# Kernel tuning notes

Hardware: AMD Instinct MI355X
Metric: run time of the kernel (lower is better)

## Reference

```python
import jax, jax.numpy as jnp
import numpy as np

C = 512

def conv1x1(x, w, b):
    # x: [B,C,H,W], w: [O,C], b: [O]
    return jnp.einsum('bchw,oc->bohw', x, w) + b[None, :, None, None]

def setup_inputs() -> dict:
    key = jax.random.key(0)
    ks = jax.random.split(key, 7)
    s = 1.0 / np.sqrt(C)
    x = jax.random.normal(ks[0], (8, C, 64, 64), dtype=jnp.float32)
    wq = jax.random.uniform(ks[1], (C, C), jnp.float32, -s, s)
    bq = jax.random.uniform(ks[2], (C,), jnp.float32, -s, s)
    wk = jax.random.uniform(ks[3], (C, C), jnp.float32, -s, s)
    bk = jax.random.uniform(ks[4], (C,), jnp.float32, -s, s)
    wv = jax.random.uniform(ks[5], (C, C), jnp.float32, -s, s)
    bv = jax.random.uniform(ks[6], (C,), jnp.float32, -s, s)
    return {"x": x, "wq": wq, "bq": bq, "wk": wk, "bk": bk, "wv": wv, "bv": bv}

def reference(x, wq, bq, wk, bk, wv, bv):
    B, Cc, H, W = x.shape
    q = conv1x1(x, wq, bq).reshape(B, Cc, H * W)   # [B,C,N]
    k = conv1x1(x, wk, bk).reshape(B, Cc, H * W)   # [B,C,N]
    v = conv1x1(x, wv, bv).reshape(B, Cc, H * W)   # [B,C,N]
    attn = jnp.einsum('bcn,bdn->bcd', q, k)        # q @ k^T over spatial dim -> [B,C,C]
    attn = jax.nn.softmax(attn, axis=-1)
    out = jnp.einsum('bcd,bdn->bcn', attn, v).reshape(B, Cc, H, W)
    return out + x
```

## Files before the change

### kernel.cpp

```cpp
#include <hip/hip_runtime.h>
#include <cstdint>

typedef unsigned short u16;
typedef unsigned int   u32;
typedef _Float16 f16;

typedef __attribute__((ext_vector_type(8))) _Float16 f16x8;
typedef __attribute__((ext_vector_type(4))) float    f32x4;

__device__ __forceinline__ u16 f2h(float f) {
    union { f16 h; u16 u; } c; c.h = (f16)f; return c.u;
}
__device__ __forceinline__ float h2f(u16 u) {
    union { u16 u; f16 h; } c; c.u = u; return (float)c.h;
}

__device__ __forceinline__ void async_copy16(const u16* g, u16* lds) {
    __builtin_amdgcn_global_load_lds(
        (const __attribute__((address_space(1))) void*)g,
        (__attribute__((address_space(3))) void*)lds,
        16, 0, 0);
}

__device__ __forceinline__ void gemm_nt_f16(
    u16* smem, const u16* __restrict__ A, int lda,
    const u16* __restrict__ B, int ldb, int K, f32x4 acc[4][4])
{
    const int t = threadIdx.x, w = t >> 6, lane = t & 63;
    const int srow = lane >> 2;
    const int skc  = (((lane & 3) ^ ((lane >> 3) & 3)) * 8);
    const int ra0 = (w*2+0)*16 + srow, ra1 = (w*2+1)*16 + srow;
    const u16* gA0 = A + (size_t)ra0 * lda + skc;
    const u16* gA1 = A + (size_t)ra1 * lda + skc;
    const u16* gB0 = B + (size_t)ra0 * ldb + skc;
    const u16* gB1 = B + (size_t)ra1 * ldb + skc;
    u16* lA0 = smem + (w*2+0)*512;
    u16* lA1 = smem + (w*2+1)*512;
    const int fr = lane & 15, fq = lane >> 4;
    const int fc = (fq ^ ((fr >> 1) & 3)) * 8;
    const int wm = (w >> 1) * 64, wn = (w & 1) * 64;
    const int fAo = (wm + fr) * 32 + fc;
    const int fBo = (wn + fr) * 32 + fc;

    for (int k0 = 0; k0 < K; k0 += 64) {
        async_copy16(gA0 + k0,      lA0);
        async_copy16(gA1 + k0,      lA1);
        async_copy16(gA0 + k0 + 32, lA0 + 4096);
        async_copy16(gA1 + k0 + 32, lA1 + 4096);
        async_copy16(gB0 + k0,      lA0 + 8192);
        async_copy16(gB1 + k0,      lA1 + 8192);
        async_copy16(gB0 + k0 + 32, lA0 + 12288);
        async_copy16(gB1 + k0 + 32, lA1 + 12288);
        __syncthreads();
        {
            f16x8 af[4], bf[4];
#pragma unroll
            for (int i = 0; i < 4; i++) af[i] = *(const f16x8*)(smem + fAo + i * 512);
#pragma unroll
            for (int i = 0; i < 4; i++) bf[i] = *(const f16x8*)(smem + 8192 + fBo + i * 512);
#pragma unroll
            for (int mi = 0; mi < 4; mi++)
#pragma unroll
                for (int ni = 0; ni < 4; ni++)
                    acc[mi][ni] = __builtin_amdgcn_mfma_f32_16x16x32_f16(
                        af[mi], bf[ni], acc[mi][ni], 0, 0, 0);
        }
        {
            f16x8 af[4], bf[4];
#pragma unroll
            for (int i = 0; i < 4; i++) af[i] = *(const f16x8*)(smem + 4096 + fAo + i * 512);
#pragma unroll
            for (int i = 0; i < 4; i++) bf[i] = *(const f16x8*)(smem + 12288 + fBo + i * 512);
#pragma unroll
            for (int mi = 0; mi < 4; mi++)
#pragma unroll
                for (int ni = 0; ni < 4; ni++)
                    acc[mi][ni] = __builtin_amdgcn_mfma_f32_16x16x32_f16(
                        af[mi], bf[ni], acc[mi][ni], 0, 0, 0);
        }
        __syncthreads();
    }
}

__device__ __forceinline__ void zero_acc(f32x4 acc[4][4]) {
#pragma unroll
    for (int i = 0; i < 4; i++)
#pragma unroll
        for (int j = 0; j < 4; j++) {
            f32x4 z = {0.f, 0.f, 0.f, 0.f};
            acc[i][j] = z;
        }
}

__global__ __launch_bounds__(256) void k_prep(const float* __restrict__ wq,
                                              const float* __restrict__ wk,
                                              const float* __restrict__ wv,
                                              u16* __restrict__ Wq2,
                                              u16* __restrict__ Wkh,
                                              u16* __restrict__ WvT,
                                              float* __restrict__ s)
{
    if (blockIdx.x < 512) {
        const int t = blockIdx.x * 256 + threadIdx.x;
        if (t < 4096) s[t] = 0.f;
        const int e = t * 4;
        const int sel = e >> 18;
        const int off = e & 262143;
        const float* src = sel ? wk : wq;
        float4 v = *(const float4*)(src + off);
        ushort4 h;
        h.x = f2h(v.x); h.y = f2h(v.y); h.z = f2h(v.z); h.w = f2h(v.w);
        if (sel == 0) {
            int i = off >> 9, c = off & 511;
            *(ushort4*)(Wq2 + (size_t)i * 1024 + c) = h;
            *(ushort4*)(Wq2 + (size_t)i * 1024 + 512 + c) = h;
        } else {
            *(ushort4*)(Wkh + off) = h;
        }
    } else {
        __shared__ u16 tile[64][70];
        const int bx = blockIdx.x - 512;
        const int t = threadIdx.x;
        const int d0 = (bx >> 3) * 64;
        const int c0 = (bx & 7) * 64;
        const int rr = t >> 4, col4 = (t & 15) * 4;
#pragma unroll
        for (int i = 0; i < 4; i++) {
            int row = i * 16 + rr;
            float4 v = *(const float4*)(wv + (size_t)(d0 + row) * 512 + c0 + col4);
            ushort4 h;
            h.x = f2h(v.x); h.y = f2h(v.y); h.z = f2h(v.z); h.w = f2h(v.w);
            *(ushort4*)&tile[row][col4] = h;
        }
        __syncthreads();
#pragma unroll
        for (int i = 0; i < 4; i++) {
            int crow = i * 16 + rr;
            ushort4 o;
            o.x = tile[col4 + 0][crow];
            o.y = tile[col4 + 1][crow];
            o.z = tile[col4 + 2][crow];
            o.w = tile[col4 + 3][crow];
            *(ushort4*)(WvT + (size_t)(c0 + crow) * 512 + d0 + col4) = o;
        }
    }
}

__global__ __launch_bounds__(256) void k_convx(const float* __restrict__ x,
                                               u16* __restrict__ Xh,
                                               u16* __restrict__ XT,
                                               float* __restrict__ s)
{
    __shared__ u16 tile[64][70];
    const int t  = threadIdx.x;
    const int b  = blockIdx.z;
    const int c0 = blockIdx.y * 64;
    const int n0 = blockIdx.x * 64;
    const int rr   = t >> 4;
    const int col4 = (t & 15) * 4;

    const float* src = x + ((size_t)b * 512 + c0) * 4096 + n0;
    u16* xh = Xh + ((size_t)b * 512 + c0) * 4096 + n0;
#pragma unroll
    for (int i = 0; i < 4; i++) {
        int row = i * 16 + rr;
        float4 v = *(const float4*)(src + (size_t)row * 4096 + col4);
        ushort4 h;
        h.x = f2h(v.x); h.y = f2h(v.y); h.z = f2h(v.z); h.w = f2h(v.w);
        *(ushort4*)&tile[row][col4] = h;
        *(ushort4*)(xh + (size_t)row * 4096 + col4) = h;
        float p = v.x + v.y + v.z + v.w;
        p += __shfl_xor(p, 1); p += __shfl_xor(p, 2);
        p += __shfl_xor(p, 4); p += __shfl_xor(p, 8);
        if ((t & 15) == 0) atomicAdd(&s[b * 512 + c0 + row], p);
    }
    __syncthreads();
    u16* dst = XT + ((size_t)b * 4096 + n0) * 512 + c0;
#pragma unroll
    for (int i = 0; i < 4; i++) {
        int nrow = i * 16 + rr;
        ushort4 o;
        o.x = tile[col4 + 0][nrow];
        o.y = tile[col4 + 1][nrow];
        o.z = tile[col4 + 2][nrow];
        o.w = tile[col4 + 3][nrow];
        *(ushort4*)(dst + (size_t)nrow * 512 + col4) = o;
    }
}

__global__ __launch_bounds__(256, 4) void k_gram(const u16* __restrict__ Xh,
                                                 float* __restrict__ Gp)
{
    __shared__ u16 smem[16384];
    const int flat = blockIdx.x;
    const int swz  = (flat & 7) * 40 + (flat >> 3);
    const int tI = swz % 10;
    const int bz = swz / 10;
    const int tm = (tI >= 9) ? 3 : (tI >= 7) ? 2 : (tI >= 4) ? 1 : 0;
    const int rs = (tm == 0) ? 0 : (tm == 1) ? 4 : (tm == 2) ? 7 : 9;
    const int tn = tI - rs + tm;
    const int m0 = tm * 128, n0 = tn * 128;
    const int b  = bz >> 2, ks = bz & 3;

    const u16* Ap = Xh + (size_t)b * 512 * 4096 + (size_t)m0 * 4096 + ks * 1024;
    const u16* Bp = Xh + (size_t)b * 512 * 4096 + (size_t)n0 * 4096 + ks * 1024;

    f32x4 acc[4][4];
    zero_acc(acc);
    gemm_nt_f16(smem, Ap, 4096, Bp, 4096, 1024, acc);

    const int t = threadIdx.x, w = t >> 6, lane = t & 63;
    const int wm = (w >> 1) * 64, wn = (w & 1) * 64;
    const int cn = lane & 15, cq = lane >> 4;

    float* base = Gp + (size_t)(ks * 8 + b) * 512 * 512;
    float* outp = base + (size_t)m0 * 512 + n0;
#pragma unroll
    for (int mi = 0; mi < 4; mi++)
#pragma unroll
        for (int ni = 0; ni < 4; ni++)
#pragma unroll
            for (int r = 0; r < 4; r++) {
                int m = wm + mi * 16 + cq * 4 + r;
                int n = wn + ni * 16 + cn;
                outp[(size_t)m * 512 + n] = acc[mi][ni][r];
            }
    if (m0 != n0) {
        float* outT = base + (size_t)n0 * 512 + m0;
#pragma unroll
        for (int mi = 0; mi < 4; mi++)
#pragma unroll
            for (int ni = 0; ni < 4; ni++) {
                int mb = wm + mi * 16 + cq * 4;
                int n  = wn + ni * 16 + cn;
                float4 v4 = { acc[mi][ni][0], acc[mi][ni][1],
                              acc[mi][ni][2], acc[mi][ni][3] };
                *(float4*)(outT + (size_t)n * 512 + mb) = v4;
            }
    }
}

__global__ __launch_bounds__(256) void k_gred(const float* __restrict__ Gp,
                                              u16* __restrict__ Ghl,
                                              const float* __restrict__ wq,
                                              const float* __restrict__ bq,
                                              const float* __restrict__ wk,
                                              const float* __restrict__ s,
                                              float* __restrict__ ubar,
                                              float* __restrict__ vv)
{
    const size_t idx = ((size_t)blockIdx.x * 256 + threadIdx.x) * 4;
    const size_t st = (size_t)8 * 512 * 512;
    float4 g0 = *(const float4*)(Gp + idx);
    float4 g1 = *(const float4*)(Gp + idx + st);
    float4 g2 = *(const float4*)(Gp + idx + 2 * st);
    float4 g3 = *(const float4*)(Gp + idx + 3 * st);
    float gx = g0.x + g1.x + g2.x + g3.x;
    float gy = g0.y + g1.y + g2.y + g3.y;
    float gz = g0.z + g1.z + g2.z + g3.z;
    float gw = g0.w + g1.w + g2.w + g3.w;
    ushort4 hi, lo;
    hi.x = f2h(gx); lo.x = f2h(gx - h2f(hi.x));
    hi.y = f2h(gy); lo.y = f2h(gy - h2f(hi.y));
    hi.z = f2h(gz); lo.z = f2h(gz - h2f(hi.z));
    hi.w = f2h(gw); lo.w = f2h(gw - h2f(hi.w));
    const size_t row = idx >> 9;
    const int c = (int)(idx & 511);
    *(ushort4*)(Ghl + row * 1024 + c) = hi;
    *(ushort4*)(Ghl + row * 1024 + 512 + c) = lo;

    if (blockIdx.x < 128) {
        const int b = blockIdx.x >> 4;
        const int sub = blockIdx.x & 15;
        const int which = sub >> 3;
        const int r0 = (sub & 7) * 64;
        const int t = threadIdx.x;
        const int i = r0 + (t >> 2), l4 = t & 3;
        const float* W = which ? wk : wq;
        const float* sb = s + b * 512;
        float acc = 0.f;
#pragma unroll 4
        for (int k = 0; k < 32; k++) {
            int c2 = k * 16 + l4 * 4;
            float4 w4 = *(const float4*)(W + (size_t)i * 512 + c2);
            float4 s4 = *(const float4*)(sb + c2);
            acc += w4.x * s4.x + w4.y * s4.y + w4.z * s4.z + w4.w * s4.w;
        }
        acc += __shfl_xor(acc, 1);
        acc += __shfl_xor(acc, 2);
        if (l4 == 0) {
            if (which) vv[b * 512 + i] = acc;
            else       ubar[b * 512 + i] = acc + 4096.0f * bq[i];
        }
    }
}

__global__ __launch_bounds__(256, 4) void k_T(const u16* __restrict__ Wq2,
                                              const u16* __restrict__ Ghl,
                                              u16* __restrict__ Tb)
{
    __shared__ u16 smem[16384];
    const int n0 = blockIdx.x * 128;
    const int m0 = blockIdx.y * 128;
    const int b  = blockIdx.z;

    const u16* Ap = Wq2 + (size_t)m0 * 1024;
    const u16* Bp = Ghl + (size_t)b * 512 * 1024 + (size_t)n0 * 1024;

    f32x4 acc[4][4];
    zero_acc(acc);
    gemm_nt_f16(smem, Ap, 1024, Bp, 1024, 1024, acc);

    const int t = threadIdx.x, w = t >> 6, lane = t & 63;
    const int wm = (w >> 1) * 64, wn = (w & 1) * 64;
    const int cn = lane & 15, cq = lane >> 4;

    u16* outp = Tb + ((size_t)b * 512 + m0) * 512 + n0;
#pragma unroll
    for (int mi = 0; mi < 4; mi++)
#pragma unroll
        for (int ni = 0; ni < 4; ni++)
#pragma unroll
            for (int r = 0; r < 4; r++) {
                int m = wm + mi * 16 + cq * 4 + r;
                int n = wn + ni * 16 + cn;
                outp[(size_t)m * 512 + n] = f2h(acc[mi][ni][r]);
            }
}

__global__ __launch_bounds__(256) void k_S(
    const u16* __restrict__ Tb, const u16* __restrict__ Wkh,
    const float* __restrict__ ubar, const float* __restrict__ vv,
    const float* __restrict__ bq, const float* __restrict__ bk,
    const float* __restrict__ bv,
    u16* __restrict__ P, float* __restrict__ pbv)
{
    __shared__ u16 smem[16896];
    __shared__ float redm[16][4];
    __shared__ float reds[16][4][2];
    u16* As = smem; u16* Bs = smem + 512;

    const int m0 = blockIdx.x * 16;
    const int b  = blockIdx.y;
    const int t = threadIdx.x, w = t >> 6, lane = t & 63;
    const int srow = lane >> 2;
    const int schunk = ((lane & 3) ^ ((srow >> 1) & 3)) * 8;
    const u16* gA = Tb + ((size_t)b * 512 + m0 + srow) * 512 + schunk;
    const int fr = lane & 15, fq = lane >> 4;
    const int fc = (fq ^ ((fr >> 1) & 3)) * 8;

    f32x4 acc[8];
#pragma unroll
    for (int i = 0; i < 8; i++) { f32x4 z = {0.f,0.f,0.f,0.f}; acc[i] = z; }

    for (int k0 = 0; k0 < 512; k0 += 32) {
        if (w == 0) async_copy16(gA + k0, As);
#pragma unroll
        for (int ii = 0; ii < 8; ii++) {
            int rbase = w * 128 + ii * 16;
            async_copy16(Wkh + (size_t)(rbase + srow) * 512 + k0 + schunk,
                         Bs + rbase * 32);
        }
        __syncthreads();
        f16x8 af = *(const f16x8*)(As + fr * 32 + fc);
#pragma unroll
        for (int ni = 0; ni < 8; ni++) {
            f16x8 bf = *(const f16x8*)(Bs + (w * 128 + ni * 16 + fr) * 32 + fc);
            acc[ni] = __builtin_amdgcn_mfma_f32_16x16x32_f16(af, bf, acc[ni], 0, 0, 0);
        }
        __syncthreads();
    }

    const int cn = lane & 15, cq = lane >> 4;
    float ub[4], bqr[4];
#pragma unroll
    for (int r = 0; r < 4; r++) {
        int i = m0 + cq * 4 + r;
        ub[r]  = ubar[b * 512 + i];
        bqr[r] = bq[i];
    }
    float vj[8], bkj[8], bvj[8];
#pragma unroll
    for (int ni = 0; ni < 8; ni++) {
        int j = w * 128 + ni * 16 + cn;
        vj[ni]  = vv[b * 512 + j];
        bkj[ni] = bk[j];
        bvj[ni] = bv[j];
    }
    float sv[8][4], mr[4];
#pragma unroll
    for (int r = 0; r < 4; r++) mr[r] = -1e30f;
#pragma unroll
    for (int ni = 0; ni < 8; ni++)
#pragma unroll
        for (int r = 0; r < 4; r++) {
            sv[ni][r] = acc[ni][r] + ub[r] * bkj[ni] + bqr[r] * vj[ni];
            mr[r] = fmaxf(mr[r], sv[ni][r]);
        }
#pragma unroll
    for (int r = 0; r < 4; r++)
        for (int o = 1; o < 16; o <<= 1) mr[r] = fmaxf(mr[r], __shfl_xor(mr[r], o));
    if (cn == 0) {
#pragma unroll
        for (int r = 0; r < 4; r++) redm[cq * 4 + r][w] = mr[r];
    }
    __syncthreads();
#pragma unroll
    for (int r = 0; r < 4; r++) {
        int row = cq * 4 + r;
        mr[r] = fmaxf(fmaxf(redm[row][0], redm[row][1]),
                      fmaxf(redm[row][2], redm[row][3]));
    }
    float e[8][4], se[4], sebv[4];
#pragma unroll
    for (int r = 0; r < 4; r++) { se[r] = 0.f; sebv[r] = 0.f; }
#pragma unroll
    for (int ni = 0; ni < 8; ni++)
#pragma unroll
        for (int r = 0; r < 4; r++) {
            float ev = __expf(sv[ni][r] - mr[r]);
            e[ni][r] = ev;
            se[r]   += ev;
            sebv[r] += ev * bvj[ni];
        }
#pragma unroll
    for (int r = 0; r < 4; r++)
        for (int o = 1; o < 16; o <<= 1) {
            se[r]   += __shfl_xor(se[r], o);
            sebv[r] += __shfl_xor(sebv[r], o);
        }
    if (cn == 0) {
#pragma unroll
        for (int r = 0; r < 4; r++) {
            reds[cq * 4 + r][w][0] = se[r];
            reds[cq * 4 + r][w][1] = sebv[r];
        }
    }
    __syncthreads();
#pragma unroll
    for (int r = 0; r < 4; r++) {
        int row = cq * 4 + r;
        float S  = reds[row][0][0] + reds[row][1][0] + reds[row][2][0] + reds[row][3][0];
        float SB = reds[row][0][1] + reds[row][1][1] + reds[row][2][1] + reds[row][3][1];
        float inv = 1.0f / S;
#pragma unroll
        for (int ni = 0; ni < 8; ni++)
            P[((size_t)b * 512 + m0 + row) * 512 + w * 128 + ni * 16 + cn] =
                f2h(e[ni][r] * inv);
        if (w == 0 && cn == 0) pbv[b * 512 + m0 + row] = SB * inv;
    }
}

__global__ __launch_bounds__(256, 4) void k_M(const u16* __restrict__ P,
                                              const u16* __restrict__ WvT,
                                              u16* __restrict__ M2)
{
    __shared__ u16 smem[16384];
    const int n0 = blockIdx.x * 128;
    const int m0 = blockIdx.y * 128;
    const int b  = blockIdx.z;

    const u16* Ap = P + (size_t)b * 512 * 512 + (size_t)m0 * 512;
    const u16* Bp = WvT + (size_t)n0 * 512;

    f32x4 acc[4][4];
    zero_acc(acc);
    gemm_nt_f16(smem, Ap, 512, Bp, 512, 512, acc);

    const int t = threadIdx.x, w = t >> 6, lane = t & 63;
    const int wm = (w >> 1) * 64, wn = (w & 1) * 64;
    const int cn = lane & 15, cq = lane >> 4;

    u16* outp = M2 + ((size_t)b * 512 + m0) * 512 + n0;
#pragma unroll
    for (int mi = 0; mi < 4; mi++)
#pragma unroll
        for (int ni = 0; ni < 4; ni++)
#pragma unroll
            for (int r = 0; r < 4; r++) {
                int m = wm + mi * 16 + cq * 4 + r;
                int n = wn + ni * 16 + cn;
                outp[(size_t)m * 512 + n] = f2h(acc[mi][ni][r]);
            }
}

__global__ __launch_bounds__(256, 4) void k_out(const u16* __restrict__ M2,
                                                const u16* __restrict__ XT,
                                                const u16* __restrict__ Xh,
                                                const float* __restrict__ pbv,
                                                float* __restrict__ out)
{
    __shared__ u16 smem[16384];
    const int flat = blockIdx.x;
    const int swz  = (flat & 7) * 128 + (flat >> 3);
    const int n0 = (swz & 31) * 128;
    const int m0 = ((swz >> 5) & 3) * 128;
    const int b  = swz >> 7;

    const u16* Ap = M2 + (size_t)b * 512 * 512 + (size_t)m0 * 512;
    const u16* Bp = XT + (size_t)b * 4096 * 512 + (size_t)n0 * 512;

    f32x4 acc[4][4];
    zero_acc(acc);
    gemm_nt_f16(smem, Ap, 512, Bp, 512, 512, acc);

    const int t = threadIdx.x, w = t >> 6, lane = t & 63;
    const int wm = (w >> 1) * 64, wn = (w & 1) * 64;
    const int cn = lane & 15, cq = lane >> 4;

#pragma unroll
    for (int mi = 0; mi < 4; mi++)
#pragma unroll
        for (int ni = 0; ni < 4; ni++)
#pragma unroll
            for (int r = 0; r < 4; r++) {
                int m = m0 + wm + mi * 16 + cq * 4 + r;
                int n = n0 + wn + ni * 16 + cn;
                size_t idx = ((size_t)b * 512 + m) * 4096 + n;
                out[idx] = acc[mi][ni][r] + pbv[b * 512 + m] + h2f(Xh[idx]);
            }
}

extern "C" void kernel_launch(void* const* d_in, const int* in_sizes, int n_in,
                              void* d_out, int out_size, void* d_ws, size_t ws_size,
                              hipStream_t stream)
{
    const float* x  = (const float*)d_in[0];
    const float* wq = (const float*)d_in[1];
    const float* bq = (const float*)d_in[2];
    const float* wk = (const float*)d_in[3];
    const float* bk = (const float*)d_in[4];
    const float* wv = (const float*)d_in[5];
    const float* bv = (const float*)d_in[6];
    float* out = (float*)d_out;

    char* ws = (char*)d_ws;
    u16*   Wq2  = (u16*)(ws);
    u16*   Wkh  = (u16*)(ws + 1048576);
    u16*   WvT  = (u16*)(ws + 1572864);
    float* s    = (float*)(ws + 2097152);
    float* ubar = (float*)(ws + 2113536);
    float* vv   = (float*)(ws + 2129920);
    float* pbv  = (float*)(ws + 2146304);
    u16*   Xh   = (u16*)(ws + 2162688);
    u16*   XT   = (u16*)(ws + 35717120);
    float* Gp   = (float*)(ws + 69271552);
    u16*   Ghl  = (u16*)(ws + 102825984);
    u16*   Tb   = (u16*)(ws + 111214592);
    u16*   P    = (u16*)(ws + 115408896);
    u16*   M2   = (u16*)(ws + 119603200);

    k_prep<<<dim3(576), dim3(256), 0, stream>>>(wq, wk, wv, Wq2, Wkh, WvT, s);
    k_convx<<<dim3(64, 8, 8), dim3(256), 0, stream>>>(x, Xh, XT, s);
    k_gram<<<dim3(320), dim3(256), 0, stream>>>(Xh, Gp);
    k_gred<<<dim3(2048), dim3(256), 0, stream>>>(Gp, Ghl, wq, bq, wk, s, ubar, vv);
    k_T<<<dim3(4, 4, 8), dim3(256), 0, stream>>>(Wq2, Ghl, Tb);
    k_S<<<dim3(32, 8), dim3(256), 0, stream>>>(Tb, Wkh, ubar, vv, bq, bk, bv, P, pbv);
    k_M<<<dim3(4, 4, 8), dim3(256), 0, stream>>>(P, WvT, M2);
    k_out<<<dim3(1024), dim3(256), 0, stream>>>(M2, XT, Xh, pbv, out);
}
```

Baseline: 250.0 us.

## Fold weight prep into gram kernel and widen softmax kernel to eight waves

Removes the separate weight-preparation launch. Its weight conversion and transpose blocks now run as extra blocks appended to the gram GEMM grid, and the accumulator zeroing becomes a memset. This hides the small prep work behind the 320 gram blocks, which alone do not fill the GPU, and removes one launch. The score/softmax kernel moves from 4 to 8 waves per block, each covering 64 columns, to get more parallelism and lower register use. The cost is a larger cross-wave reduction, and the gram kernel may use more registers because of the added branches.

```diff
diff --git a/kernel.cpp b/kernel.cpp
--- a/kernel.cpp
+++ b/kernel.cpp
@@ -92,17 +92,107 @@
         }
 }
 
-__global__ __launch_bounds__(256) void k_prep(const float* __restrict__ wq,
-                                              const float* __restrict__ wk,
-                                              const float* __restrict__ wv,
-                                              u16* __restrict__ Wq2,
-                                              u16* __restrict__ Wkh,
-                                              u16* __restrict__ WvT,
-                                              float* __restrict__ s)
-{
-    if (blockIdx.x < 512) {
-        const int t = blockIdx.x * 256 + threadIdx.x;
-        if (t < 4096) s[t] = 0.f;
+__global__ __launch_bounds__(256) void k_convx(const float* __restrict__ x,
+                                               u16* __restrict__ Xh,
+                                               u16* __restrict__ XT,
+                                               float* __restrict__ s)
+{
+    __shared__ u16 tile[64][70];
+    const int t  = threadIdx.x;
+    const int b  = blockIdx.z;
+    const int c0 = blockIdx.y * 64;
+    const int n0 = blockIdx.x * 64;
+    const int rr   = t >> 4;
+    const int col4 = (t & 15) * 4;
+
+    const float* src = x + ((size_t)b * 512 + c0) * 4096 + n0;
+    u16* xh = Xh + ((size_t)b * 512 + c0) * 4096 + n0;
+#pragma unroll
+    for (int i = 0; i < 4; i++) {
+        int row = i * 16 + rr;
+        float4 v = *(const float4*)(src + (size_t)row * 4096 + col4);
+        ushort4 h;
+        h.x = f2h(v.x); h.y = f2h(v.y); h.z = f2h(v.z); h.w = f2h(v.w);
+        *(ushort4*)&tile[row][col4] = h;
+        *(ushort4*)(xh + (size_t)row * 4096 + col4) = h;
+        float p = v.x + v.y + v.z + v.w;
+        p += __shfl_xor(p, 1); p += __shfl_xor(p, 2);
+        p += __shfl_xor(p, 4); p += __shfl_xor(p, 8);
+        if ((t & 15) == 0) atomicAdd(&s[b * 512 + c0 + row], p);
+    }
+    __syncthreads();
+    u16* dst = XT + ((size_t)b * 4096 + n0) * 512 + c0;
+#pragma unroll
+    for (int i = 0; i < 4; i++) {
+        int nrow = i * 16 + rr;
+        ushort4 o;
+        o.x = tile[col4 + 0][nrow];
+        o.y = tile[col4 + 1][nrow];
+        o.z = tile[col4 + 2][nrow];
+        o.w = tile[col4 + 3][nrow];
+        *(ushort4*)(dst + (size_t)nrow * 512 + col4) = o;
+    }
+}
+
+__global__ __launch_bounds__(256, 4) void k_gram(const u16* __restrict__ Xh,
+                                                 float* __restrict__ Gp,
+                                                 const float* __restrict__ wq,
+                                                 const float* __restrict__ wk,
+                                                 const float* __restrict__ wv,
+                                                 u16* __restrict__ Wq2,
+                                                 u16* __restrict__ Wkh,
+                                                 u16* __restrict__ WvT)
+{
+    __shared__ u16 smem[16384];
+    const int bxx = blockIdx.x;
+    if (bxx < 320) {
+        const int swz  = (bxx & 7) * 40 + (bxx >> 3);
+        const int tI = swz % 10;
+        const int bz = swz / 10;
+        const int tm = (tI >= 9) ? 3 : (tI >= 7) ? 2 : (tI >= 4) ? 1 : 0;
+        const int rs = (tm == 0) ? 0 : (tm == 1) ? 4 : (tm == 2) ? 7 : 9;
+        const int tn = tI - rs + tm;
+        const int m0 = tm * 128, n0 = tn * 128;
+        const int b  = bz >> 2, ks = bz & 3;
+
+        const u16* Ap = Xh + (size_t)b * 512 * 4096 + (size_t)m0 * 4096 + ks * 1024;
+        const u16* Bp = Xh + (size_t)b * 512 * 4096 + (size_t)n0 * 4096 + ks * 1024;
+
+        f32x4 acc[4][4];
+        zero_acc(acc);
+        gemm_nt_f16(smem, Ap, 4096, Bp, 4096, 1024, acc);
+
+        const int t = threadIdx.x, w = t >> 6, lane = t & 63;
+        const int wm = (w >> 1) * 64, wn = (w & 1) * 64;
+        const int cn = lane & 15, cq = lane >> 4;
+
+        float* base = Gp + (size_t)(ks * 8 + b) * 512 * 512;
+        float* outp = base + (size_t)m0 * 512 + n0;
+#pragma unroll
+        for (int mi = 0; mi < 4; mi++)
+#pragma unroll
+            for (int ni = 0; ni < 4; ni++)
+#pragma unroll
+                for (int r = 0; r < 4; r++) {
+                    int m = wm + mi * 16 + cq * 4 + r;
+                    int n = wn + ni * 16 + cn;
+                    outp[(size_t)m * 512 + n] = acc[mi][ni][r];
+                }
+        if (m0 != n0) {
+            float* outT = base + (size_t)n0 * 512 + m0;
+#pragma unroll
+            for (int mi = 0; mi < 4; mi++)
+#pragma unroll
+                for (int ni = 0; ni < 4; ni++) {
+                    int mb = wm + mi * 16 + cq * 4;
+                    int n  = wn + ni * 16 + cn;
+                    float4 v4 = { acc[mi][ni][0], acc[mi][ni][1],
+                                  acc[mi][ni][2], acc[mi][ni][3] };
+                    *(float4*)(outT + (size_t)n * 512 + mb) = v4;
+                }
+        }
+    } else if (bxx < 832) {
+        const int t = (bxx - 320) * 256 + threadIdx.x;
         const int e = t * 4;
         const int sel = e >> 18;
         const int off = e & 262143;
@@ -118,8 +208,8 @@
             *(ushort4*)(Wkh + off) = h;
         }
     } else {
-        __shared__ u16 tile[64][70];
-        const int bx = blockIdx.x - 512;
+        u16 (*tile)[70] = (u16(*)[70])smem;
+        const int bx = bxx - 832;
         const int t = threadIdx.x;
         const int d0 = (bx >> 3) * 64;
         const int c0 = (bx & 7) * 64;
@@ -143,100 +233,6 @@
             o.w = tile[col4 + 3][crow];
             *(ushort4*)(WvT + (size_t)(c0 + crow) * 512 + d0 + col4) = o;
         }
-    }
-}
-
-__global__ __launch_bounds__(256) void k_convx(const float* __restrict__ x,
-                                               u16* __restrict__ Xh,
-                                               u16* __restrict__ XT,
-                                               float* __restrict__ s)
-{
-    __shared__ u16 tile[64][70];
-    const int t  = threadIdx.x;
-    const int b  = blockIdx.z;
-    const int c0 = blockIdx.y * 64;
-    const int n0 = blockIdx.x * 64;
-    const int rr   = t >> 4;
-    const int col4 = (t & 15) * 4;
-
-    const float* src = x + ((size_t)b * 512 + c0) * 4096 + n0;
-    u16* xh = Xh + ((size_t)b * 512 + c0) * 4096 + n0;
-#pragma unroll
-    for (int i = 0; i < 4; i++) {
-        int row = i * 16 + rr;
-        float4 v = *(const float4*)(src + (size_t)row * 4096 + col4);
-        ushort4 h;
-        h.x = f2h(v.x); h.y = f2h(v.y); h.z = f2h(v.z); h.w = f2h(v.w);
-        *(ushort4*)&tile[row][col4] = h;
-        *(ushort4*)(xh + (size_t)row * 4096 + col4) = h;
-        float p = v.x + v.y + v.z + v.w;
-        p += __shfl_xor(p, 1); p += __shfl_xor(p, 2);
-        p += __shfl_xor(p, 4); p += __shfl_xor(p, 8);
-        if ((t & 15) == 0) atomicAdd(&s[b * 512 + c0 + row], p);
-    }
-    __syncthreads();
-    u16* dst = XT + ((size_t)b * 4096 + n0) * 512 + c0;
-#pragma unroll
-    for (int i = 0; i < 4; i++) {
-        int nrow = i * 16 + rr;
-        ushort4 o;
-        o.x = tile[col4 + 0][nrow];
-        o.y = tile[col4 + 1][nrow];
-        o.z = tile[col4 + 2][nrow];
-        o.w = tile[col4 + 3][nrow];
-        *(ushort4*)(dst + (size_t)nrow * 512 + col4) = o;
-    }
-}
-
-__global__ __launch_bounds__(256, 4) void k_gram(const u16* __restrict__ Xh,
-                                                 float* __restrict__ Gp)
-{
-    __shared__ u16 smem[16384];
-    const int flat = blockIdx.x;
-    const int swz  = (flat & 7) * 40 + (flat >> 3);
-    const int tI = swz % 10;
-    const int bz = swz / 10;
-    const int tm = (tI >= 9) ? 3 : (tI >= 7) ? 2 : (tI >= 4) ? 1 : 0;
-    const int rs = (tm == 0) ? 0 : (tm == 1) ? 4 : (tm == 2) ? 7 : 9;
-    const int tn = tI - rs + tm;
-    const int m0 = tm * 128, n0 = tn * 128;
-    const int b  = bz >> 2, ks = bz & 3;
-
-    const u16* Ap = Xh + (size_t)b * 512 * 4096 + (size_t)m0 * 4096 + ks * 1024;
-    const u16* Bp = Xh + (size_t)b * 512 * 4096 + (size_t)n0 * 4096 + ks * 1024;
-
-    f32x4 acc[4][4];
-    zero_acc(acc);
-    gemm_nt_f16(smem, Ap, 4096, Bp, 4096, 1024, acc);
-
-    const int t = threadIdx.x, w = t >> 6, lane = t & 63;
-    const int wm = (w >> 1) * 64, wn = (w & 1) * 64;
-    const int cn = lane & 15, cq = lane >> 4;
-
-    float* base = Gp + (size_t)(ks * 8 + b) * 512 * 512;
-    float* outp = base + (size_t)m0 * 512 + n0;
-#pragma unroll
-    for (int mi = 0; mi < 4; mi++)
-#pragma unroll
-        for (int ni = 0; ni < 4; ni++)
-#pragma unroll
-            for (int r = 0; r < 4; r++) {
-                int m = wm + mi * 16 + cq * 4 + r;
-                int n = wn + ni * 16 + cn;
-                outp[(size_t)m * 512 + n] = acc[mi][ni][r];
-            }
-    if (m0 != n0) {
-        float* outT = base + (size_t)n0 * 512 + m0;
-#pragma unroll
-        for (int mi = 0; mi < 4; mi++)
-#pragma unroll
-            for (int ni = 0; ni < 4; ni++) {
-                int mb = wm + mi * 16 + cq * 4;
-                int n  = wn + ni * 16 + cn;
-                float4 v4 = { acc[mi][ni][0], acc[mi][ni][1],
-                              acc[mi][ni][2], acc[mi][ni][3] };
-                *(float4*)(outT + (size_t)n * 512 + mb) = v4;
-            }
     }
 }
 
@@ -328,17 +324,17 @@
             }
 }
 
-__global__ __launch_bounds__(256) void k_S(
+__global__ __launch_bounds__(512) void k_S(
     const u16* __restrict__ Tb, const u16* __restrict__ Wkh,
     const float* __restrict__ ubar, const float* __restrict__ vv,
     const float* __restrict__ bq, const float* __restrict__ bk,
     const float* __restrict__ bv,
     u16* __restrict__ P, float* __restrict__ pbv)
 {
-    __shared__ u16 smem[16896];
-    __shared__ float redm[16][4];
-    __shared__ float reds[16][4][2];
-    u16* As = smem; u16* Bs = smem + 512;
+    __shared__ u16 As[512];
+    __shared__ u16 Bs[16384];
+    __shared__ float redm[16][8];
+    __shared__ float reds[16][8][2];
 
     const int m0 = blockIdx.x * 16;
     const int b  = blockIdx.y;
@@ -349,23 +345,23 @@
     const int fr = lane & 15, fq = lane >> 4;
     const int fc = (fq ^ ((fr >> 1) & 3)) * 8;
 
-    f32x4 acc[8];
-#pragma unroll
-    for (int i = 0; i < 8; i++) { f32x4 z = {0.f,0.f,0.f,0.f}; acc[i] = z; }
+    f32x4 acc[4];
+#pragma unroll
+    for (int i = 0; i < 4; i++) { f32x4 z = {0.f,0.f,0.f,0.f}; acc[i] = z; }
 
     for (int k0 = 0; k0 < 512; k0 += 32) {
         if (w == 0) async_copy16(gA + k0, As);
 #pragma unroll
-        for (int ii = 0; ii < 8; ii++) {
-            int rbase = w * 128 + ii * 16;
+        for (int ii = 0; ii < 4; ii++) {
+            int rbase = w * 64 + ii * 16;
             async_copy16(Wkh + (size_t)(rbase + srow) * 512 + k0 + schunk,
                          Bs + rbase * 32);
         }
         __syncthreads();
         f16x8 af = *(const f16x8*)(As + fr * 32 + fc);
 #pragma unroll
-        for (int ni = 0; ni < 8; ni++) {
-            f16x8 bf = *(const f16x8*)(Bs + (w * 128 + ni * 16 + fr) * 32 + fc);
+        for (int ni = 0; ni < 4; ni++) {
+            f16x8 bf = *(const f16x8*)(Bs + (w * 64 + ni * 16 + fr) * 32 + fc);
             acc[ni] = __builtin_amdgcn_mfma_f32_16x16x32_f16(af, bf, acc[ni], 0, 0, 0);
         }
         __syncthreads();
@@ -379,19 +375,19 @@
         ub[r]  = ubar[b * 512 + i];
         bqr[r] = bq[i];
     }
-    float vj[8], bkj[8], bvj[8];
-#pragma unroll
-    for (int ni = 0; ni < 8; ni++) {
-        int j = w * 128 + ni * 16 + cn;
+    float vj[4], bkj[4], bvj[4];
+#pragma unroll
+    for (int ni = 0; ni < 4; ni++) {
+        int j = w * 64 + ni * 16 + cn;
         vj[ni]  = vv[b * 512 + j];
         bkj[ni] = bk[j];
         bvj[ni] = bv[j];
     }
-    float sv[8][4], mr[4];
+    float sv[4][4], mr[4];
 #pragma unroll
     for (int r = 0; r < 4; r++) mr[r] = -1e30f;
 #pragma unroll
-    for (int ni = 0; ni < 8; ni++)
+    for (int ni = 0; ni < 4; ni++)
 #pragma unroll
         for (int r = 0; r < 4; r++) {
             sv[ni][r] = acc[ni][r] + ub[r] * bkj[ni] + bqr[r] * vj[ni];
@@ -408,14 +404,17 @@
 #pragma unroll
     for (int r = 0; r < 4; r++) {
         int row = cq * 4 + r;
-        mr[r] = fmaxf(fmaxf(redm[row][0], redm[row][1]),
-                      fmaxf(redm[row][2], redm[row][3]));
-    }
-    float e[8][4], se[4], sebv[4];
+        float m01 = fmaxf(redm[row][0], redm[row][1]);
+        float m23 = fmaxf(redm[row][2], redm[row][3]);
+        float m45 = fmaxf(redm[row][4], redm[row][5]);
+        float m67 = fmaxf(redm[row][6], redm[row][7]);
+        mr[r] = fmaxf(fmaxf(m01, m23), fmaxf(m45, m67));
+    }
+    float e[4][4], se[4], sebv[4];
 #pragma unroll
     for (int r = 0; r < 4; r++) { se[r] = 0.f; sebv[r] = 0.f; }
 #pragma unroll
-    for (int ni = 0; ni < 8; ni++)
+    for (int ni = 0; ni < 4; ni++)
 #pragma unroll
         for (int r = 0; r < 4; r++) {
             float ev = __expf(sv[ni][r] - mr[r]);
@@ -440,12 +439,16 @@
 #pragma unroll
     for (int r = 0; r < 4; r++) {
         int row = cq * 4 + r;
-        float S  = reds[row][0][0] + reds[row][1][0] + reds[row][2][0] + reds[row][3][0];
-        float SB = reds[row][0][1] + reds[row][1][1] + reds[row][2][1] + reds[row][3][1];
+        float S = 0.f, SB = 0.f;
+#pragma unroll
+        for (int ww = 0; ww < 8; ww++) {
+            S  += reds[row][ww][0];
+            SB += reds[row][ww][1];
+        }
         float inv = 1.0f / S;
 #pragma unroll
-        for (int ni = 0; ni < 8; ni++)
-            P[((size_t)b * 512 + m0 + row) * 512 + w * 128 + ni * 16 + cn] =
+        for (int ni = 0; ni < 4; ni++)
+            P[((size_t)b * 512 + m0 + row) * 512 + w * 64 + ni * 16 + cn] =
                 f2h(e[ni][r] * inv);
         if (w == 0 && cn == 0) pbv[b * 512 + m0 + row] = SB * inv;
     }
@@ -550,12 +553,12 @@
     u16*   P    = (u16*)(ws + 115408896);
     u16*   M2   = (u16*)(ws + 119603200);
 
-    k_prep<<<dim3(576), dim3(256), 0, stream>>>(wq, wk, wv, Wq2, Wkh, WvT, s);
+    hipMemsetAsync(s, 0, 4096 * sizeof(float), stream);
     k_convx<<<dim3(64, 8, 8), dim3(256), 0, stream>>>(x, Xh, XT, s);
-    k_gram<<<dim3(320), dim3(256), 0, stream>>>(Xh, Gp);
+    k_gram<<<dim3(896), dim3(256), 0, stream>>>(Xh, Gp, wq, wk, wv, Wq2, Wkh, WvT);
     k_gred<<<dim3(2048), dim3(256), 0, stream>>>(Gp, Ghl, wq, bq, wk, s, ubar, vv);
     k_T<<<dim3(4, 4, 8), dim3(256), 0, stream>>>(Wq2, Ghl, Tb);
-    k_S<<<dim3(32, 8), dim3(256), 0, stream>>>(Tb, Wkh, ubar, vv, bq, bk, bv, P, pbv);
+    k_S<<<dim3(32, 8), dim3(512), 0, stream>>>(Tb, Wkh, ubar, vv, bq, bk, bv, P, pbv);
     k_M<<<dim3(4, 4, 8), dim3(256), 0, stream>>>(P, WvT, M2);
     k_out<<<dim3(1024), dim3(256), 0, stream>>>(M2, XT, Xh, pbv, out);
 }
```

After: 247.7 us. No clear change (-0.9%).
